# Optimization experiments

Hardware: AMD Instinct MI355X
Metric: run time of the kernel (lower is better)

The kernel has to match this reference:

```python
import jax, jax.numpy as jnp
import numpy as np

N = 50000
E = 1600000
D_IN, D_H1, D_H2 = 256, 128, 64


def setup_inputs() -> dict:
    key = jax.random.key(0)
    ks = jax.random.split(key, 16)
    def lin(k, fan_in, fan_out):
        # torch nn.Linear default init: U(-1/sqrt(fan_in), 1/sqrt(fan_in))
        kw, kb = jax.random.split(k)
        bound = 1.0 / np.sqrt(fan_in)
        W = jax.random.uniform(kw, (fan_out, fan_in), jnp.float32, -bound, bound)
        b = jax.random.uniform(kb, (fan_out,), jnp.float32, -bound, bound)
        return W, b
    x = jax.random.normal(ks[0], (N, D_IN), jnp.float32)
    edge_index = jax.random.randint(ks[1], (2, E), 0, N, jnp.int64)
    edge_weight = jax.random.uniform(ks[2], (E,), jnp.float32)
    enc1_w, enc1_b = lin(ks[3], D_IN, D_H1)
    enc2_w, enc2_b = lin(ks[4], D_H1, D_H2)
    gcn1_w, gcn1_b = lin(ks[5], D_H2, D_H2)
    gcn2_w, gcn2_b = lin(ks[6], D_H2, D_H2)
    dec1_w, dec1_b = lin(ks[7], D_H2, D_H1)
    dec2_w, dec2_b = lin(ks[8], D_H1, D_IN)
    return dict(x=x, edge_index=edge_index, edge_weight=edge_weight,
                enc1_w=enc1_w, enc1_b=enc1_b, enc2_w=enc2_w, enc2_b=enc2_b,
                gcn1_w=gcn1_w, gcn1_b=gcn1_b, gcn2_w=gcn2_w, gcn2_b=gcn2_b,
                dec1_w=dec1_w, dec1_b=dec1_b, dec2_w=dec2_w, dec2_b=dec2_b)


def _gcn_conv(h, src, dst, w_all, W, b, n_nodes):
    # PyG GCNConv: h' = D^{-1/2}(A+I)D^{-1/2} (h W^T) + b; self-loops already in src/dst/w_all
    h = h @ W.T
    deg = jax.ops.segment_sum(w_all, dst, num_segments=n_nodes)
    dinv = jnp.where(deg > 0, jax.lax.rsqrt(jnp.maximum(deg, 1e-12)), 0.0)
    norm = dinv[src] * w_all * dinv[dst]                 # [E+N]
    msg = h[src] * norm[:, None]                         # gather + scale
    out = jax.ops.segment_sum(msg, dst, num_segments=n_nodes)  # scatter-add
    return out + b


def reference(x, edge_index, edge_weight,
              enc1_w, enc1_b, enc2_w, enc2_b,
              gcn1_w, gcn1_b, gcn2_w, gcn2_b,
              dec1_w, dec1_b, dec2_w, dec2_b):
    n = x.shape[0]
    # add self-loops (weight 1.0), as PyG GCNConv does by default
    loop = jnp.arange(n, dtype=edge_index.dtype)
    src = jnp.concatenate([edge_index[0], loop])
    dst = jnp.concatenate([edge_index[1], loop])
    w_all = jnp.concatenate([edge_weight, jnp.ones((n,), edge_weight.dtype)])

    h = jax.nn.relu(x @ enc1_w.T + enc1_b)
    h = jax.nn.relu(h @ enc2_w.T + enc2_b)
    h = jax.nn.relu(_gcn_conv(h, src, dst, w_all, gcn1_w, gcn1_b, n))
    h = jax.nn.relu(_gcn_conv(h, src, dst, w_all, gcn2_w, gcn2_b, n))
    h = jax.nn.relu(h @ dec1_w.T + dec1_b)
    h = h @ dec2_w.T + dec2_b
    return jax.nn.sigmoid(h)
```

## Files before the change

### kernel.cpp

```cpp
#include <hip/hip_runtime.h>


constexpr int NBLK = 128;
constexpr int GRP  = NBLK / 8;

typedef __attribute__((ext_vector_type(8))) short bf16x8;
typedef __attribute__((ext_vector_type(4))) float f32x4;

__device__ inline void split2(float f0, float f1, unsigned& hp, unsigned& lp) {
    unsigned u0 = __float_as_uint(f0), u1 = __float_as_uint(f1);
    hp = (u1 & 0xFFFF0000u) | (u0 >> 16);
    float r0 = f0 - __uint_as_float(u0 & 0xFFFF0000u);
    float r1 = f1 - __uint_as_float(u1 & 0xFFFF0000u);
    lp = (__float_as_uint(r1) & 0xFFFF0000u) | (__float_as_uint(r0) >> 16);
}

template <int K, int M, int ACT, bool BIAS>
__global__ __launch_bounds__(256) void gemm_mf(const float* __restrict__ A,
                                               const float* __restrict__ W,
                                               const float* __restrict__ bias,
                                               float* __restrict__ C, int N) {
    static_assert(K % 64 == 0, "K%64");
    constexpr int KC = 64;
    __shared__ unsigned Ah[128][36];
    __shared__ unsigned Al[128][36];
    __shared__ unsigned Wh[64][36];
    __shared__ unsigned Wl[64][36];

    const int tid      = threadIdx.x;
    const int nodeBase = blockIdx.x * 128;
    const int foff     = blockIdx.y * 64;

    const int srow = tid >> 4;
    const int sc4  = tid & 15;
    float4 av[8];
    float4 wv[4];

#pragma unroll
    for (int q = 0; q < 8; ++q) {
        const int r  = q * 16 + srow;
        const int gn = nodeBase + r;
        av[q] = (gn < N) ? *(const float4*)(A + (size_t)gn * K + sc4 * 4)
                         : make_float4(0.f, 0.f, 0.f, 0.f);
    }
#pragma unroll
    for (int q = 0; q < 4; ++q) {
        const int r = q * 16 + srow;
        wv[q] = *(const float4*)(W + (size_t)(foff + r) * K + sc4 * 4);
    }

    f32x4 acc[4][2];
#pragma unroll
    for (int mf = 0; mf < 4; ++mf)
#pragma unroll
        for (int nf = 0; nf < 2; ++nf) acc[mf][nf] = (f32x4)0.f;

    const int lane = tid & 63;
    const int wid  = tid >> 6;
    const int wm   = wid >> 1;
    const int wn   = wid & 1;
    const int fr   = lane & 15;
    const int fg   = lane >> 4;

    for (int kc = 0; kc < K; kc += KC) {
#pragma unroll
        for (int q = 0; q < 8; ++q) {
            unsigned h0, l0, h1, l1;
            split2(av[q].x, av[q].y, h0, l0);
            split2(av[q].z, av[q].w, h1, l1);
            const int r = q * 16 + srow;
            Ah[r][sc4 * 2] = h0; Ah[r][sc4 * 2 + 1] = h1;
            Al[r][sc4 * 2] = l0; Al[r][sc4 * 2 + 1] = l1;
        }
#pragma unroll
        for (int q = 0; q < 4; ++q) {
            unsigned h0, l0, h1, l1;
            split2(wv[q].x, wv[q].y, h0, l0);
            split2(wv[q].z, wv[q].w, h1, l1);
            const int r = q * 16 + srow;
            Wh[r][sc4 * 2] = h0; Wh[r][sc4 * 2 + 1] = h1;
            Wl[r][sc4 * 2] = l0; Wl[r][sc4 * 2 + 1] = l1;
        }
        __syncthreads();

        if (kc + KC < K) {
#pragma unroll
            for (int q = 0; q < 8; ++q) {
                const int r  = q * 16 + srow;
                const int gn = nodeBase + r;
                av[q] = (gn < N)
                    ? *(const float4*)(A + (size_t)gn * K + kc + KC + sc4 * 4)
                    : make_float4(0.f, 0.f, 0.f, 0.f);
            }
#pragma unroll
            for (int q = 0; q < 4; ++q) {
                const int r = q * 16 + srow;
                wv[q] = *(const float4*)(W + (size_t)(foff + r) * K + kc + KC + sc4 * 4);
            }
        }

#pragma unroll
        for (int kf = 0; kf < 2; ++kf) {
            bf16x8 ah[4], alo[4], bh[2], blo[2];
#pragma unroll
            for (int mf = 0; mf < 4; ++mf) {
                const int r = wm * 64 + mf * 16 + fr;
                ah[mf]  = *(const bf16x8*)&Ah[r][kf * 16 + fg * 4];
                alo[mf] = *(const bf16x8*)&Al[r][kf * 16 + fg * 4];
            }
#pragma unroll
            for (int nf = 0; nf < 2; ++nf) {
                const int r = wn * 32 + nf * 16 + fr;
                bh[nf]  = *(const bf16x8*)&Wh[r][kf * 16 + fg * 4];
                blo[nf] = *(const bf16x8*)&Wl[r][kf * 16 + fg * 4];
            }
#pragma unroll
            for (int mf = 0; mf < 4; ++mf)
#pragma unroll
                for (int nf = 0; nf < 2; ++nf) {
                    acc[mf][nf] = __builtin_amdgcn_mfma_f32_16x16x32_bf16(
                        ah[mf], bh[nf], acc[mf][nf], 0, 0, 0);
                    acc[mf][nf] = __builtin_amdgcn_mfma_f32_16x16x32_bf16(
                        alo[mf], bh[nf], acc[mf][nf], 0, 0, 0);
                    acc[mf][nf] = __builtin_amdgcn_mfma_f32_16x16x32_bf16(
                        ah[mf], blo[nf], acc[mf][nf], 0, 0, 0);
                }
        }
        __syncthreads();
    }

#pragma unroll
    for (int nf = 0; nf < 2; ++nf) {
        const int feat = foff + wn * 32 + nf * 16 + fr;
        const float bv = BIAS ? bias[feat] : 0.f;
#pragma unroll
        for (int mf = 0; mf < 4; ++mf) {
            const int node0 = nodeBase + wm * 64 + mf * 16 + fg * 4;
#pragma unroll
            for (int i = 0; i < 4; ++i) {
                const int node = node0 + i;
                if (node < N) {
                    float x = acc[mf][nf][i] + bv;
                    if constexpr (ACT == 1) x = fmaxf(x, 0.f);
                    if constexpr (ACT == 2) x = 1.f / (1.f + __expf(-x));
                    C[(size_t)node * M + feat] = x;
                }
            }
        }
    }
}


__global__ __launch_bounds__(256) void count_k(const int* __restrict__ ei,
                                               int* __restrict__ cnt,
                                               int NB, int E) {
    __shared__ int hist[784];
    const int tid = threadIdx.x;
    for (int i = tid; i < NB; i += 256) hist[i] = 0;
    __syncthreads();
    const int chunk = (E + NBLK - 1) / NBLK;
    const int lo = blockIdx.x * chunk;
    const int hi = min(lo + chunk, E);
    for (int e = lo + tid; e < hi; e += 256) {
        int d = ei[E + e];
        atomicAdd(&hist[d >> 6], 1);
    }
    __syncthreads();
    const int r = blockIdx.x & 7, g = blockIdx.x >> 3;
    for (int i = tid; i < NB; i += 256)
        cnt[i * NBLK + r * GRP + g] = hist[i];
}

__global__ __launch_bounds__(256) void scan1(const int* __restrict__ cnt,
                                             int* __restrict__ pos,
                                             int* __restrict__ bs, int n) {
    __shared__ int s[256];
    const int t = threadIdx.x;
    const int i0 = blockIdx.x * 512 + 2 * t;
    int c0 = (i0     < n) ? cnt[i0]     : 0;
    int c1 = (i0 + 1 < n) ? cnt[i0 + 1] : 0;
    int c = c0 + c1;
    s[t] = c;
    __syncthreads();
    for (int off = 1; off < 256; off <<= 1) {
        int v = (t >= off) ? s[t - off] : 0;
        __syncthreads();
        s[t] += v;
        __syncthreads();
    }
    int excl = s[t] - c;
    if (i0     < n) pos[i0]     = excl;
    if (i0 + 1 < n) pos[i0 + 1] = excl + c0;
    if (t == 255) bs[blockIdx.x] = s[255];
}

__global__ __launch_bounds__(256) void scan_tops(int* __restrict__ bs, int nb) {
    __shared__ int s[256];
    int t = threadIdx.x;
    int v = (t < nb) ? bs[t] : 0;
    s[t] = v;
    __syncthreads();
    for (int off = 1; off < 256; off <<= 1) {
        int u = (t >= off) ? s[t - off] : 0;
        __syncthreads();
        s[t] += u;
        __syncthreads();
    }
    if (t < nb) bs[t] = s[t] - v;
}

__global__ __launch_bounds__(256) void scan2(int* __restrict__ pos,
                                             const int* __restrict__ bs,
                                             int* __restrict__ bucketBase,
                                             int n, int NB, int E) {
    const int t = threadIdx.x;
    const int i0 = blockIdx.x * 512 + 2 * t;
    const int add = bs[blockIdx.x];
#pragma unroll
    for (int c = 0; c < 2; ++c) {
        int i = i0 + c;
        if (i < n) {
            int v = pos[i] + add;
            pos[i] = v;
            if ((i & (NBLK - 1)) == 0) bucketBase[i >> 7] = v;
        }
    }
    if (blockIdx.x == 0 && t == 0) bucketBase[NB] = E;
}

__global__ __launch_bounds__(256) void place_k(const int* __restrict__ ei,
                                               const float* __restrict__ w,
                                               const int* __restrict__ pos,
                                               int2* __restrict__ ebuf,
                                               int NB, int E) {
    __shared__ int cur[784];
    const int tid = threadIdx.x;
    const int r = blockIdx.x & 7, g = blockIdx.x >> 3;
    for (int i = tid; i < NB; i += 256) cur[i] = pos[i * NBLK + r * GRP + g];
    __syncthreads();
    const int chunk = (E + NBLK - 1) / NBLK;
    const int lo = blockIdx.x * chunk;
    const int hi = min(lo + chunk, E);
    for (int e = lo + tid; e < hi; e += 256) {
        int s = ei[e];
        int d = ei[E + e];
        float wv = w[e];
        int p = atomicAdd(&cur[d >> 6], 1);
        ebuf[p] = make_int2(s | ((d & 63) << 26), __float_as_int(wv));
    }
}

__global__ __launch_bounds__(256) void bucket_build(const int2* __restrict__ ebuf,
                                                    const int* __restrict__ bucketBase,
                                                    int2* __restrict__ sn,
                                                    int* __restrict__ row,
                                                    float* __restrict__ dinv,
                                                    int N, int E) {
    __shared__ int   lh[64];
    __shared__ float ldg[64];
    __shared__ int   sc[64];
    __shared__ int   lofs[64];
    const int tid  = threadIdx.x;
    const int base = bucketBase[blockIdx.x];
    const int end  = bucketBase[blockIdx.x + 1];

    if (tid < 64) { lh[tid] = 0; ldg[tid] = 0.f; }
    __syncthreads();
    for (int i = base + tid; i < end; i += 256) {
        int2 v = ebuf[i];
        int dl = ((unsigned)v.x) >> 26;
        atomicAdd(&lh[dl], 1);
        atomicAdd(&ldg[dl], __int_as_float(v.y));
    }
    __syncthreads();
    if (tid < 64) sc[tid] = lh[tid];
    __syncthreads();
    for (int off = 1; off < 64; off <<= 1) {
        int v = (tid < 64 && tid >= off) ? sc[tid - off] : 0;
        __syncthreads();
        if (tid < 64) sc[tid] += v;
        __syncthreads();
    }
    if (tid < 64) {
        int excl = sc[tid] - lh[tid];
        int d = (blockIdx.x << 6) + tid;
        if (d < N) {
            row[d]  = base + excl;
            dinv[d] = rsqrtf(fmaxf(1.0f + ldg[tid], 1e-12f));
        }
        lofs[tid] = base + excl;
    }
    __syncthreads();
    for (int i = base + tid; i < end; i += 256) {
        int2 v = ebuf[i];
        unsigned u = (unsigned)v.x;
        int dl = u >> 26;
        int s  = u & 0x03FFFFFF;
        int p  = atomicAdd(&lofs[dl], 1);
        sn[p] = make_int2(s, v.y);
    }
    if (blockIdx.x == 0 && tid == 0) row[N] = E;
}

__global__ __launch_bounds__(256) void scale_pay(int2* __restrict__ sn,
                                                 const float* __restrict__ dinv,
                                                 int E) {
    int p = blockIdx.x * 256 + threadIdx.x;
    if (p < E) {
        int2 v = sn[p];
        sn[p] = make_int2(v.x, __float_as_int(__int_as_float(v.y) * dinv[v.x]));
    }
}

__global__ __launch_bounds__(256) void gcn_agg(const float* __restrict__ t,
                                               const int2* __restrict__ sn,
                                               const int* __restrict__ row,
                                               const float* __restrict__ dinv,
                                               const float* __restrict__ bias,
                                               float* __restrict__ out, int N) {
    const int lane = threadIdx.x & 63;
    int i = __builtin_amdgcn_readfirstlane((int)(blockIdx.x * 4) + (threadIdx.x >> 6));
    if (i >= N) return;
    float di   = dinv[i];
    float self = t[(size_t)i * 64 + lane];
    float acc  = 0.f;
    int p  = row[i];
    int pe = row[i + 1];
    for (; p + 4 <= pe; p += 4) {
        int2 v0 = sn[p];
        int2 v1 = sn[p + 1];
        int2 v2 = sn[p + 2];
        int2 v3 = sn[p + 3];
        acc += t[(size_t)v0.x * 64 + lane] * __int_as_float(v0.y);
        acc += t[(size_t)v1.x * 64 + lane] * __int_as_float(v1.y);
        acc += t[(size_t)v2.x * 64 + lane] * __int_as_float(v2.y);
        acc += t[(size_t)v3.x * 64 + lane] * __int_as_float(v3.y);
    }
    for (; p < pe; ++p) {
        int2 v = sn[p];
        acc += t[(size_t)v.x * 64 + lane] * __int_as_float(v.y);
    }
    float x = (acc + self * di) * di + bias[lane];
    out[(size_t)i * 64 + lane] = fmaxf(x, 0.f);
}

extern "C" void kernel_launch(void* const* d_in, const int* in_sizes, int n_in,
                              void* d_out, int out_size, void* d_ws, size_t ws_size,
                              hipStream_t stream) {
    const float* x      = (const float*)d_in[0];
    const int*   ei     = (const int*)d_in[1];
    const float* ew     = (const float*)d_in[2];
    const float* enc1_w = (const float*)d_in[3];
    const float* enc1_b = (const float*)d_in[4];
    const float* enc2_w = (const float*)d_in[5];
    const float* enc2_b = (const float*)d_in[6];
    const float* gcn1_w = (const float*)d_in[7];
    const float* gcn1_b = (const float*)d_in[8];
    const float* gcn2_w = (const float*)d_in[9];
    const float* gcn2_b = (const float*)d_in[10];
    const float* dec1_w = (const float*)d_in[11];
    const float* dec1_b = (const float*)d_in[12];
    const float* dec2_w = (const float*)d_in[13];
    const float* dec2_b = (const float*)d_in[14];

    const int N  = in_sizes[0] / 256;
    const int E  = in_sizes[2];
    const int NB = (N + 63) / 64;
    const int NCNT = NB * NBLK;
    const int NS   = (NCNT + 511) / 512;

    float* ws   = (float*)d_ws;
    float* bufA = ws;
    int2*  sn   = (int2*)bufA;
    float* bufC = bufA + (size_t)2 * E;
    int2*  ebuf = (int2*)bufC;
    float* bufB = bufA + (size_t)N * 128;
    float* dinv = bufB + (size_t)N * 64;
    int*   row  = (int*)(dinv + N);
    int*   cnt  = row + (N + 1);
    int*   pos  = cnt + NCNT;
    int*   bucketBase = pos + NCNT;
    int*   bs   = bucketBase + (NB + 1);

    const int gemmGrid = (N + 127) / 128;
    const int nBlkE    = (E + 255) / 256;

    gemm_mf<256, 128, 1, true><<<dim3(gemmGrid, 2), 256, 0, stream>>>(
        x, enc1_w, enc1_b, bufA, N);
    gemm_mf<128, 64, 1, true><<<dim3(gemmGrid, 1), 256, 0, stream>>>(
        bufA, enc2_w, enc2_b, bufB, N);

    count_k<<<NBLK, 256, 0, stream>>>(ei, cnt, NB, E);
    scan1<<<NS, 256, 0, stream>>>(cnt, pos, bs, NCNT);
    scan_tops<<<1, 256, 0, stream>>>(bs, NS);
    scan2<<<NS, 256, 0, stream>>>(pos, bs, bucketBase, NCNT, NB, E);
    place_k<<<NBLK, 256, 0, stream>>>(ei, ew, pos, ebuf, NB, E);
    bucket_build<<<NB, 256, 0, stream>>>(ebuf, bucketBase, sn, row, dinv, N, E);
    scale_pay<<<nBlkE, 256, 0, stream>>>(sn, dinv, E);

    gemm_mf<64, 64, 0, false><<<dim3(gemmGrid, 1), 256, 0, stream>>>(
        bufB, gcn1_w, nullptr, bufC, N);
    gcn_agg<<<(N + 3) / 4, 256, 0, stream>>>(bufC, sn, row, dinv, gcn1_b, bufB, N);

    gemm_mf<64, 64, 0, false><<<dim3(gemmGrid, 1), 256, 0, stream>>>(
        bufB, gcn2_w, nullptr, bufC, N);
    gcn_agg<<<(N + 3) / 4, 256, 0, stream>>>(bufC, sn, row, dinv, gcn2_b, bufB, N);

    gemm_mf<64, 128, 1, true><<<dim3(gemmGrid, 2), 256, 0, stream>>>(
        bufB, dec1_w, dec1_b, bufA, N);
    gemm_mf<128, 256, 2, true><<<dim3(gemmGrid, 4), 256, 0, stream>>>(
        bufA, dec2_w, dec2_b, (float*)d_out, N);
}
```

Measured before the change: 462.1 us.

## Pre-split weights to bf16 hi/lo once and widen GEMM N tiles

Adds a single kernel that splits all six weight matrices into bf16 high/low halves up front. The GEMMs then read the pre-split weights straight from global memory into registers, skipping the per-block weight split and its LDS staging. GEMM tiles become templated so a block covers 128 or 64 output features, which halves or removes the grid's feature dimension and cuts how often the activation matrix is re-read and re-split. The cost is one extra launch plus uncoalesced per-lane global weight loads that depend on cache hits, and more accumulator registers per wave.

```diff
diff --git a/kernel.cpp b/kernel.cpp
--- a/kernel.cpp
+++ b/kernel.cpp
@@ -15,50 +15,63 @@
     lp = (__float_as_uint(r1) & 0xFFFF0000u) | (__float_as_uint(r0) >> 16);
 }
 
-template <int K, int M, int ACT, bool BIAS>
-__global__ __launch_bounds__(256) void gemm_mf(const float* __restrict__ A,
-                                               const float* __restrict__ W,
+struct WSplitArgs {
+    const float* src[6];
+    unsigned short* hi[6];
+    unsigned short* lo[6];
+    int n[6];
+};
+__global__ __launch_bounds__(256) void split_w(WSplitArgs a) {
+    const int L = blockIdx.y;
+    const int i = blockIdx.x * 256 + threadIdx.x;
+    if (i < a.n[L]) {
+        float f = a.src[L][i];
+        unsigned u = __float_as_uint(f);
+        float r = f - __uint_as_float(u & 0xFFFF0000u);
+        a.hi[L][i] = (unsigned short)(u >> 16);
+        a.lo[L][i] = (unsigned short)(__float_as_uint(r) >> 16);
+    }
+}
+
+template <int K, int M, int ACT, bool BIAS, int WM, int WN, int MF, int NF>
+__global__ __launch_bounds__(256) void gemm_bd(const float* __restrict__ A,
+                                               const unsigned short* __restrict__ Whp,
+                                               const unsigned short* __restrict__ Wlp,
                                                const float* __restrict__ bias,
                                                float* __restrict__ C, int N) {
     static_assert(K % 64 == 0, "K%64");
+    static_assert(WM * WN == 4, "4 waves");
+    static_assert(WM * MF * 16 == 128, "BM=128");
     constexpr int KC = 64;
+    constexpr int BN = WN * NF * 16;
     __shared__ unsigned Ah[128][36];
     __shared__ unsigned Al[128][36];
-    __shared__ unsigned Wh[64][36];
-    __shared__ unsigned Wl[64][36];
 
     const int tid      = threadIdx.x;
     const int nodeBase = blockIdx.x * 128;
-    const int foff     = blockIdx.y * 64;
+    const int foff     = blockIdx.y * BN;
 
     const int srow = tid >> 4;
     const int sc4  = tid & 15;
     float4 av[8];
-    float4 wv[4];
 
 #pragma unroll
     for (int q = 0; q < 8; ++q) {
-        const int r  = q * 16 + srow;
-        const int gn = nodeBase + r;
+        const int gn = nodeBase + q * 16 + srow;
         av[q] = (gn < N) ? *(const float4*)(A + (size_t)gn * K + sc4 * 4)
                          : make_float4(0.f, 0.f, 0.f, 0.f);
     }
-#pragma unroll
-    for (int q = 0; q < 4; ++q) {
-        const int r = q * 16 + srow;
-        wv[q] = *(const float4*)(W + (size_t)(foff + r) * K + sc4 * 4);
-    }
-
-    f32x4 acc[4][2];
-#pragma unroll
-    for (int mf = 0; mf < 4; ++mf)
-#pragma unroll
-        for (int nf = 0; nf < 2; ++nf) acc[mf][nf] = (f32x4)0.f;
+
+    f32x4 acc[MF][NF];
+#pragma unroll
+    for (int mf = 0; mf < MF; ++mf)
+#pragma unroll
+        for (int nf = 0; nf < NF; ++nf) acc[mf][nf] = (f32x4)0.f;
 
     const int lane = tid & 63;
     const int wid  = tid >> 6;
-    const int wm   = wid >> 1;
-    const int wn   = wid & 1;
+    const int wm   = wid / WN;
+    const int wn   = wid % WN;
     const int fr   = lane & 15;
     const int fg   = lane >> 4;
 
@@ -72,70 +85,57 @@
             Ah[r][sc4 * 2] = h0; Ah[r][sc4 * 2 + 1] = h1;
             Al[r][sc4 * 2] = l0; Al[r][sc4 * 2 + 1] = l1;
         }
-#pragma unroll
-        for (int q = 0; q < 4; ++q) {
-            unsigned h0, l0, h1, l1;
-            split2(wv[q].x, wv[q].y, h0, l0);
-            split2(wv[q].z, wv[q].w, h1, l1);
-            const int r = q * 16 + srow;
-            Wh[r][sc4 * 2] = h0; Wh[r][sc4 * 2 + 1] = h1;
-            Wl[r][sc4 * 2] = l0; Wl[r][sc4 * 2 + 1] = l1;
-        }
         __syncthreads();
 
         if (kc + KC < K) {
 #pragma unroll
             for (int q = 0; q < 8; ++q) {
-                const int r  = q * 16 + srow;
-                const int gn = nodeBase + r;
+                const int gn = nodeBase + q * 16 + srow;
                 av[q] = (gn < N)
                     ? *(const float4*)(A + (size_t)gn * K + kc + KC + sc4 * 4)
                     : make_float4(0.f, 0.f, 0.f, 0.f);
             }
-#pragma unroll
-            for (int q = 0; q < 4; ++q) {
-                const int r = q * 16 + srow;
-                wv[q] = *(const float4*)(W + (size_t)(foff + r) * K + kc + KC + sc4 * 4);
+        }
+
+#pragma unroll
+        for (int kf = 0; kf < 2; ++kf) {
+            bf16x8 bh[NF], bl[NF];
+#pragma unroll
+            for (int nf = 0; nf < NF; ++nf) {
+                const size_t wo = (size_t)(foff + wn * NF * 16 + nf * 16 + fr) * K
+                                  + kc + kf * 32 + fg * 8;
+                bh[nf] = *(const bf16x8*)(Whp + wo);
+                bl[nf] = *(const bf16x8*)(Wlp + wo);
             }
-        }
-
-#pragma unroll
-        for (int kf = 0; kf < 2; ++kf) {
-            bf16x8 ah[4], alo[4], bh[2], blo[2];
-#pragma unroll
-            for (int mf = 0; mf < 4; ++mf) {
-                const int r = wm * 64 + mf * 16 + fr;
+            bf16x8 ah[MF], alo[MF];
+#pragma unroll
+            for (int mf = 0; mf < MF; ++mf) {
+                const int r = wm * MF * 16 + mf * 16 + fr;
                 ah[mf]  = *(const bf16x8*)&Ah[r][kf * 16 + fg * 4];
                 alo[mf] = *(const bf16x8*)&Al[r][kf * 16 + fg * 4];
             }
 #pragma unroll
-            for (int nf = 0; nf < 2; ++nf) {
-                const int r = wn * 32 + nf * 16 + fr;
-                bh[nf]  = *(const bf16x8*)&Wh[r][kf * 16 + fg * 4];
-                blo[nf] = *(const bf16x8*)&Wl[r][kf * 16 + fg * 4];
-            }
-#pragma unroll
-            for (int mf = 0; mf < 4; ++mf)
-#pragma unroll
-                for (int nf = 0; nf < 2; ++nf) {
+            for (int mf = 0; mf < MF; ++mf)
+#pragma unroll
+                for (int nf = 0; nf < NF; ++nf) {
                     acc[mf][nf] = __builtin_amdgcn_mfma_f32_16x16x32_bf16(
                         ah[mf], bh[nf], acc[mf][nf], 0, 0, 0);
                     acc[mf][nf] = __builtin_amdgcn_mfma_f32_16x16x32_bf16(
                         alo[mf], bh[nf], acc[mf][nf], 0, 0, 0);
                     acc[mf][nf] = __builtin_amdgcn_mfma_f32_16x16x32_bf16(
-                        ah[mf], blo[nf], acc[mf][nf], 0, 0, 0);
+                        ah[mf], bl[nf], acc[mf][nf], 0, 0, 0);
                 }
         }
         __syncthreads();
     }
 
 #pragma unroll
-    for (int nf = 0; nf < 2; ++nf) {
-        const int feat = foff + wn * 32 + nf * 16 + fr;
+    for (int nf = 0; nf < NF; ++nf) {
+        const int feat = foff + wn * NF * 16 + nf * 16 + fr;
         const float bv = BIAS ? bias[feat] : 0.f;
 #pragma unroll
-        for (int mf = 0; mf < 4; ++mf) {
-            const int node0 = nodeBase + wm * 64 + mf * 16 + fg * 4;
+        for (int mf = 0; mf < MF; ++mf) {
+            const int node0 = nodeBase + wm * MF * 16 + mf * 16 + fg * 4;
 #pragma unroll
             for (int i = 0; i < 4; ++i) {
                 const int node = node0 + i;
@@ -381,14 +381,28 @@
     int*   pos  = cnt + NCNT;
     int*   bucketBase = pos + NCNT;
     int*   bs   = bucketBase + (NB + 1);
+    unsigned short* whi = (unsigned short*)(bs + 256);
+    unsigned short* wlo = whi + 90112;
 
     const int gemmGrid = (N + 127) / 128;
     const int nBlkE    = (E + 255) / 256;
 
-    gemm_mf<256, 128, 1, true><<<dim3(gemmGrid, 2), 256, 0, stream>>>(
-        x, enc1_w, enc1_b, bufA, N);
-    gemm_mf<128, 64, 1, true><<<dim3(gemmGrid, 1), 256, 0, stream>>>(
-        bufA, enc2_w, enc2_b, bufB, N);
+    WSplitArgs wa;
+    const float* wsrc[6] = {enc1_w, enc2_w, gcn1_w, gcn2_w, dec1_w, dec2_w};
+    const int    wsz[6]  = {32768, 8192, 4096, 4096, 8192, 32768};
+    const int    woff[6] = {0, 32768, 40960, 45056, 49152, 57344};
+    for (int l = 0; l < 6; ++l) {
+        wa.src[l] = wsrc[l];
+        wa.hi[l]  = whi + woff[l];
+        wa.lo[l]  = wlo + woff[l];
+        wa.n[l]   = wsz[l];
+    }
+    split_w<<<dim3(128, 6), 256, 0, stream>>>(wa);
+
+    gemm_bd<256, 128, 1, true, 2, 2, 4, 4><<<dim3(gemmGrid, 1), 256, 0, stream>>>(
+        x, whi + woff[0], wlo + woff[0], enc1_b, bufA, N);
+    gemm_bd<128, 64, 1, true, 4, 1, 2, 4><<<dim3(gemmGrid, 1), 256, 0, stream>>>(
+        bufA, whi + woff[1], wlo + woff[1], enc2_b, bufB, N);
 
     count_k<<<NBLK, 256, 0, stream>>>(ei, cnt, NB, E);
     scan1<<<NS, 256, 0, stream>>>(cnt, pos, bs, NCNT);
@@ -398,16 +412,16 @@
     bucket_build<<<NB, 256, 0, stream>>>(ebuf, bucketBase, sn, row, dinv, N, E);
     scale_pay<<<nBlkE, 256, 0, stream>>>(sn, dinv, E);
 
-    gemm_mf<64, 64, 0, false><<<dim3(gemmGrid, 1), 256, 0, stream>>>(
-        bufB, gcn1_w, nullptr, bufC, N);
+    gemm_bd<64, 64, 0, false, 4, 1, 2, 4><<<dim3(gemmGrid, 1), 256, 0, stream>>>(
+        bufB, whi + woff[2], wlo + woff[2], nullptr, bufC, N);
     gcn_agg<<<(N + 3) / 4, 256, 0, stream>>>(bufC, sn, row, dinv, gcn1_b, bufB, N);
 
-    gemm_mf<64, 64, 0, false><<<dim3(gemmGrid, 1), 256, 0, stream>>>(
-        bufB, gcn2_w, nullptr, bufC, N);
+    gemm_bd<64, 64, 0, false, 4, 1, 2, 4><<<dim3(gemmGrid, 1), 256, 0, stream>>>(
+        bufB, whi + woff[3], wlo + woff[3], nullptr, bufC, N);
     gcn_agg<<<(N + 3) / 4, 256, 0, stream>>>(bufC, sn, row, dinv, gcn2_b, bufB, N);
 
-    gemm_mf<64, 128, 1, true><<<dim3(gemmGrid, 2), 256, 0, stream>>>(
-        bufB, dec1_w, dec1_b, bufA, N);
-    gemm_mf<128, 256, 2, true><<<dim3(gemmGrid, 4), 256, 0, stream>>>(
-        bufA, dec2_w, dec2_b, (float*)d_out, N);
-}
+    gemm_bd<64, 128, 1, true, 2, 2, 4, 4><<<dim3(gemmGrid, 1), 256, 0, stream>>>(
+        bufB, whi + woff[4], wlo + woff[4], dec1_b, bufA, N);
+    gemm_bd<128, 256, 2, true, 2, 2, 4, 4><<<dim3(gemmGrid, 2), 256, 0, stream>>>(
+        bufA, whi + woff[5], wlo + woff[5], dec2_b, (float*)d_out, N);
+}
```

New measurement: 468.7 us. No clear change (+1.4%).

## Rewrite GEMMs to stage fp32 A tiles via async global-to-LDS DMA

Applied to the files above, without the earlier changes.

Replaces the register-staged GEMM, which split A and W into bf16 hi/lo halves before storing them to LDS, with a kernel that DMAs raw fp32 A tiles into double-buffered, XOR-swizzled LDS using global_load_lds. The bf16 split now happens after reading from LDS, and W fragments are loaded straight from global memory per k-step. Tiles shrink from 128 to 64 nodes, and the grid is reordered so blocks sharing a node tile are adjacent. This aims to overlap loads with MFMA work and improve occupancy, at the cost of redundant split work and repeated uncached-in-LDS W loads.

```diff
diff --git a/kernel.cpp b/kernel.cpp
--- a/kernel.cpp
+++ b/kernel.cpp
@@ -15,118 +15,102 @@
     lp = (__float_as_uint(r1) & 0xFFFF0000u) | (__float_as_uint(r0) >> 16);
 }
 
+struct Bf16Pair { bf16x8 h, l; };
+__device__ inline Bf16Pair split8(float4 a, float4 b) {
+    union { unsigned u[4]; bf16x8 v; } H, L;
+    split2(a.x, a.y, H.u[0], L.u[0]);
+    split2(a.z, a.w, H.u[1], L.u[1]);
+    split2(b.x, b.y, H.u[2], L.u[2]);
+    split2(b.z, b.w, H.u[3], L.u[3]);
+    Bf16Pair p; p.h = H.v; p.l = L.v; return p;
+}
+
+__device__ __forceinline__ void dma16(const float* g, void* l) {
+    __builtin_amdgcn_global_load_lds(
+        (const __attribute__((address_space(1))) unsigned*)g,
+        (__attribute__((address_space(3))) unsigned*)l, 16, 0, 0);
+}
+
 template <int K, int M, int ACT, bool BIAS>
-__global__ __launch_bounds__(256) void gemm_mf(const float* __restrict__ A,
-                                               const float* __restrict__ W,
-                                               const float* __restrict__ bias,
-                                               float* __restrict__ C, int N) {
+__global__ __launch_bounds__(256) void gemm_dma(const float* __restrict__ A,
+                                                const float* __restrict__ W,
+                                                const float* __restrict__ bias,
+                                                float* __restrict__ C, int N) {
     static_assert(K % 64 == 0, "K%64");
-    constexpr int KC = 64;
-    __shared__ unsigned Ah[128][36];
-    __shared__ unsigned Al[128][36];
-    __shared__ unsigned Wh[64][36];
-    __shared__ unsigned Wl[64][36];
+    constexpr int KS = 64;
+    __shared__ __align__(16) unsigned char Ab[2][16384];
 
     const int tid      = threadIdx.x;
-    const int nodeBase = blockIdx.x * 128;
-    const int foff     = blockIdx.y * 64;
-
-    const int srow = tid >> 4;
-    const int sc4  = tid & 15;
-    float4 av[8];
-    float4 wv[4];
-
-#pragma unroll
-    for (int q = 0; q < 8; ++q) {
-        const int r  = q * 16 + srow;
-        const int gn = nodeBase + r;
-        av[q] = (gn < N) ? *(const float4*)(A + (size_t)gn * K + sc4 * 4)
-                         : make_float4(0.f, 0.f, 0.f, 0.f);
-    }
-#pragma unroll
-    for (int q = 0; q < 4; ++q) {
-        const int r = q * 16 + srow;
-        wv[q] = *(const float4*)(W + (size_t)(foff + r) * K + sc4 * 4);
-    }
-
-    f32x4 acc[4][2];
-#pragma unroll
-    for (int mf = 0; mf < 4; ++mf)
+    const int lane     = tid & 63;
+    const int wid      = tid >> 6;
+    const int wm       = wid >> 1;
+    const int wn       = wid & 1;
+    const int fr       = lane & 15;
+    const int fg       = lane >> 4;
+    const int foff     = blockIdx.x * 64;
+    const int nodeBase = blockIdx.y * 64;
+
+    auto STAGE = [&](int buf, int kc) {
+#pragma unroll
+        for (int c = 0; c < 4; ++c) {
+            const int chunk = (wid * 4 + c) * 1024;
+            const int s     = chunk + lane * 16;
+            const int r     = s >> 8;
+            const int si    = (s & 255) ^ ((r & 7) << 4);
+            int row = nodeBase + r;
+            if (row >= N) row = N - 1;
+            const float* gp = A + (size_t)row * K + kc + (si >> 2);
+            dma16(gp, (char*)Ab[buf] + chunk);
+        }
+    };
+
+    f32x4 acc[2][2];
+#pragma unroll
+    for (int mf = 0; mf < 2; ++mf)
 #pragma unroll
         for (int nf = 0; nf < 2; ++nf) acc[mf][nf] = (f32x4)0.f;
 
-    const int lane = tid & 63;
-    const int wid  = tid >> 6;
-    const int wm   = wid >> 1;
-    const int wn   = wid & 1;
-    const int fr   = lane & 15;
-    const int fg   = lane >> 4;
-
-    for (int kc = 0; kc < K; kc += KC) {
-#pragma unroll
-        for (int q = 0; q < 8; ++q) {
-            unsigned h0, l0, h1, l1;
-            split2(av[q].x, av[q].y, h0, l0);
-            split2(av[q].z, av[q].w, h1, l1);
-            const int r = q * 16 + srow;
-            Ah[r][sc4 * 2] = h0; Ah[r][sc4 * 2 + 1] = h1;
-            Al[r][sc4 * 2] = l0; Al[r][sc4 * 2 + 1] = l1;
-        }
-#pragma unroll
-        for (int q = 0; q < 4; ++q) {
-            unsigned h0, l0, h1, l1;
-            split2(wv[q].x, wv[q].y, h0, l0);
-            split2(wv[q].z, wv[q].w, h1, l1);
-            const int r = q * 16 + srow;
-            Wh[r][sc4 * 2] = h0; Wh[r][sc4 * 2 + 1] = h1;
-            Wl[r][sc4 * 2] = l0; Wl[r][sc4 * 2 + 1] = l1;
-        }
-        __syncthreads();
-
-        if (kc + KC < K) {
-#pragma unroll
-            for (int q = 0; q < 8; ++q) {
-                const int r  = q * 16 + srow;
-                const int gn = nodeBase + r;
-                av[q] = (gn < N)
-                    ? *(const float4*)(A + (size_t)gn * K + kc + KC + sc4 * 4)
-                    : make_float4(0.f, 0.f, 0.f, 0.f);
+    STAGE(0, 0);
+    int cur = 0;
+    for (int kc = 0; kc < K; kc += KS) {
+        __syncthreads();
+        if (kc + KS < K) STAGE(cur ^ 1, kc + KS);
+
+#pragma unroll
+        for (int kf = 0; kf < 2; ++kf) {
+            bf16x8 ah[2], al[2], bh[2], bl[2];
+#pragma unroll
+            for (int mf = 0; mf < 2; ++mf) {
+                const int r  = wm * 32 + mf * 16 + fr;
+                const int xr = (r & 7) << 4;
+                const int ch = kf * 8 + fg * 2;
+                float4 f0 = *(const float4*)&Ab[cur][r * 256 + ((ch * 16) ^ xr)];
+                float4 f1 = *(const float4*)&Ab[cur][r * 256 + (((ch + 1) * 16) ^ xr)];
+                Bf16Pair p = split8(f0, f1);
+                ah[mf] = p.h; al[mf] = p.l;
             }
 #pragma unroll
-            for (int q = 0; q < 4; ++q) {
-                const int r = q * 16 + srow;
-                wv[q] = *(const float4*)(W + (size_t)(foff + r) * K + kc + KC + sc4 * 4);
+            for (int nf = 0; nf < 2; ++nf) {
+                const float* wp = W + (size_t)(foff + wn * 32 + nf * 16 + fr) * K
+                                  + kc + kf * 32 + fg * 8;
+                float4 g0 = *(const float4*)wp;
+                float4 g1 = *(const float4*)(wp + 4);
+                Bf16Pair p = split8(g0, g1);
+                bh[nf] = p.h; bl[nf] = p.l;
             }
-        }
-
-#pragma unroll
-        for (int kf = 0; kf < 2; ++kf) {
-            bf16x8 ah[4], alo[4], bh[2], blo[2];
-#pragma unroll
-            for (int mf = 0; mf < 4; ++mf) {
-                const int r = wm * 64 + mf * 16 + fr;
-                ah[mf]  = *(const bf16x8*)&Ah[r][kf * 16 + fg * 4];
-                alo[mf] = *(const bf16x8*)&Al[r][kf * 16 + fg * 4];
-            }
-#pragma unroll
-            for (int nf = 0; nf < 2; ++nf) {
-                const int r = wn * 32 + nf * 16 + fr;
-                bh[nf]  = *(const bf16x8*)&Wh[r][kf * 16 + fg * 4];
-                blo[nf] = *(const bf16x8*)&Wl[r][kf * 16 + fg * 4];
-            }
-#pragma unroll
-            for (int mf = 0; mf < 4; ++mf)
+#pragma unroll
+            for (int mf = 0; mf < 2; ++mf)
 #pragma unroll
                 for (int nf = 0; nf < 2; ++nf) {
                     acc[mf][nf] = __builtin_amdgcn_mfma_f32_16x16x32_bf16(
                         ah[mf], bh[nf], acc[mf][nf], 0, 0, 0);
                     acc[mf][nf] = __builtin_amdgcn_mfma_f32_16x16x32_bf16(
-                        alo[mf], bh[nf], acc[mf][nf], 0, 0, 0);
+                        al[mf], bh[nf], acc[mf][nf], 0, 0, 0);
                     acc[mf][nf] = __builtin_amdgcn_mfma_f32_16x16x32_bf16(
-                        ah[mf], blo[nf], acc[mf][nf], 0, 0, 0);
+                        ah[mf], bl[nf], acc[mf][nf], 0, 0, 0);
                 }
         }
-        __syncthreads();
+        cur ^= 1;
     }
 
 #pragma unroll
@@ -134,8 +118,8 @@
         const int feat = foff + wn * 32 + nf * 16 + fr;
         const float bv = BIAS ? bias[feat] : 0.f;
 #pragma unroll
-        for (int mf = 0; mf < 4; ++mf) {
-            const int node0 = nodeBase + wm * 64 + mf * 16 + fg * 4;
+        for (int mf = 0; mf < 2; ++mf) {
+            const int node0 = nodeBase + wm * 32 + mf * 16 + fg * 4;
 #pragma unroll
             for (int i = 0; i < 4; ++i) {
                 const int node = node0 + i;
@@ -382,12 +366,12 @@
     int*   bucketBase = pos + NCNT;
     int*   bs   = bucketBase + (NB + 1);
 
-    const int gemmGrid = (N + 127) / 128;
-    const int nBlkE    = (E + 255) / 256;
-
-    gemm_mf<256, 128, 1, true><<<dim3(gemmGrid, 2), 256, 0, stream>>>(
+    const int nodeTiles = (N + 63) / 64;
+    const int nBlkE     = (E + 255) / 256;
+
+    gemm_dma<256, 128, 1, true><<<dim3(2, nodeTiles), 256, 0, stream>>>(
         x, enc1_w, enc1_b, bufA, N);
-    gemm_mf<128, 64, 1, true><<<dim3(gemmGrid, 1), 256, 0, stream>>>(
+    gemm_dma<128, 64, 1, true><<<dim3(1, nodeTiles), 256, 0, stream>>>(
         bufA, enc2_w, enc2_b, bufB, N);
 
     count_k<<<NBLK, 256, 0, stream>>>(ei, cnt, NB, E);
@@ -398,16 +382,16 @@
     bucket_build<<<NB, 256, 0, stream>>>(ebuf, bucketBase, sn, row, dinv, N, E);
     scale_pay<<<nBlkE, 256, 0, stream>>>(sn, dinv, E);
 
-    gemm_mf<64, 64, 0, false><<<dim3(gemmGrid, 1), 256, 0, stream>>>(
+    gemm_dma<64, 64, 0, false><<<dim3(1, nodeTiles), 256, 0, stream>>>(
         bufB, gcn1_w, nullptr, bufC, N);
     gcn_agg<<<(N + 3) / 4, 256, 0, stream>>>(bufC, sn, row, dinv, gcn1_b, bufB, N);
 
-    gemm_mf<64, 64, 0, false><<<dim3(gemmGrid, 1), 256, 0, stream>>>(
+    gemm_dma<64, 64, 0, false><<<dim3(1, nodeTiles), 256, 0, stream>>>(
         bufB, gcn2_w, nullptr, bufC, N);
     gcn_agg<<<(N + 3) / 4, 256, 0, stream>>>(bufC, sn, row, dinv, gcn2_b, bufB, N);
 
-    gemm_mf<64, 128, 1, true><<<dim3(gemmGrid, 2), 256, 0, stream>>>(
+    gemm_dma<64, 128, 1, true><<<dim3(2, nodeTiles), 256, 0, stream>>>(
         bufB, dec1_w, dec1_b, bufA, N);
-    gemm_mf<128, 256, 2, true><<<dim3(gemmGrid, 4), 256, 0, stream>>>(
+    gemm_dma<128, 256, 2, true><<<dim3(4, nodeTiles), 256, 0, stream>>>(
         bufA, dec2_w, dec2_b, (float*)d_out, N);
 }
```

Result: no change. 465.3 us (+0.7%).
